# Kernel optimization log

Hardware: AMD Instinct MI355X
Metric: run time of the kernel (lower is better)

Reference implementation:

```python
import jax, jax.numpy as jnp
import numpy as np

B, A_IN, C_IN, H, W_ = 8, 16, 4, 64, 64   # batch, input atoms, input capsules, spatial
K, C_OUT, A_OUT, ROUTINGS = 5, 8, 32, 3
EPS = 1e-7


def setup_inputs() -> dict:
    key = jax.random.key(0)
    k1, k2 = jax.random.split(key)
    x = jax.random.normal(k1, (B, A_IN, C_IN, H, W_), dtype=jnp.float32)
    # kaiming_uniform_(fan_in, relu): bound = sqrt(3) * sqrt(2) / sqrt(fan_in)
    fan_in = A_IN * K * K
    bound = float(np.sqrt(6.0 / fan_in))
    W = jax.random.uniform(k2, (C_OUT * A_OUT, A_IN, K, K), jnp.float32, -bound, bound)
    b = jnp.full((1, 1, C_OUT, A_OUT), 0.1, dtype=jnp.float32)
    return {"x": x, "W": W, "b": b}


def _squash(v):
    # v: (..., atoms); SegCaps squash with epsilon inside sqrt
    sq = jnp.sum(v * v, axis=-1, keepdims=True)
    return v * (sq / (1.0 + sq) / jnp.sqrt(sq + EPS))


def reference(x, W, b):
    # Faithful to torch: permute then raw row-major reshapes (byte reinterpret)
    t = jnp.transpose(x, (2, 0, 3, 4, 1))                      # (C_IN, B, H, W, A_IN)
    t = t.reshape(C_IN * B, H, W_, A_IN).reshape(-1, A_IN, H, W_)
    conv = jax.lax.conv_general_dilated(
        t, W, window_strides=(1, 1), padding="SAME",
        dimension_numbers=("NCHW", "OIHW", "NCHW"))             # (C_IN*B, C_OUT*A_OUT, h, w)
    ch, cw = conv.shape[2], conv.shape[3]
    votes = conv.reshape(B, C_IN, ch, cw, C_OUT, A_OUT)         # raw reinterpret, as in torch
    biases = jnp.tile(b, (ch, cw, 1, 1))                        # (h, w, C_OUT, A_OUT)

    # dynamic routing (SegCaps update_routing)
    logits = jnp.zeros((B, C_IN, ch, cw, C_OUT), dtype=votes.dtype)
    activation = None
    for _ in range(ROUTINGS):
        route = jax.nn.softmax(logits, axis=-1)                 # (B, Cin, h, w, Cout)
        preact = jnp.einsum("bihwo,bihwoa->bhwoa", route, votes) + biases
        activation = _squash(preact)                            # (B, h, w, Cout, A)
        agreement = jnp.einsum("bihwoa,bhwoa->bihwo", votes, activation)
        logits = logits + agreement
    return jnp.transpose(activation, (0, 4, 3, 1, 2))           # (B, A_OUT, C_OUT, h, w)
```

## Files before the change

kernel.cpp:

```cpp
#include <hip/hip_runtime.h>
#include <hip/hip_bf16.h>


typedef _Float16 half8 __attribute__((ext_vector_type(8)));
typedef _Float16 half4v __attribute__((ext_vector_type(4)));
typedef float floatx4 __attribute__((ext_vector_type(4)));

#define EPSF 1e-7f

__global__ __launch_bounds__(256) void k_pack2(const float* __restrict__ x,
                                               _Float16* __restrict__ th) {
  __shared__ float lin[32 * 306 + 18];
  const int bid = blockIdx.x;
  const int n   = bid >> 3;
  const int a0h = (bid >> 2) & 1;
  const int W0  = (bid & 3) * 16;
  const int ci = n >> 3, b0 = n & 7;
  const int tid = threadIdx.x;
  const float* xb = x + b0 * 262144 + ci * 4096 + W0;

  for (int p = 0; p < 8; ++p) {
    int rr = p * 64 + (tid >> 2);
    int q  = (tid & 3) * 4;
    int a1 = rr >> 5, m = rr & 31;
    float4 v = *(const float4*)(xb + a1 * 16384 + (a0h * 32 + m) * 64 + q);
    float* d = lin + m * 306 + a1 * 18 + q;
    d[0] = v.x; d[1] = v.y; d[2] = v.z; d[3] = v.w;
  }
  __syncthreads();

  _Float16* tb = th + (size_t)n * 65536 + a0h * 32768 + W0 * 128;
  for (int hh = 0; hh < 4; ++hh) {
    int w1 = tid >> 4, a1 = tid & 15;
    half8 v;
#pragma unroll
    for (int j = 0; j < 8; ++j)
      v[j] = (_Float16)lin[(j * 4 + hh) * 306 + a1 * 18 + w1];
    *(half8*)(tb + hh * 8192 + w1 * 128 + a1 * 8) = v;
  }
}

__global__ __launch_bounds__(256) void k_packw(const float* __restrict__ W,
                                               _Float16* __restrict__ Wp) {
  int id = blockIdx.x * 256 + threadIdx.x;
  int a  = id & 15;
  int oc = (id >> 4) & 255;
  int kk = id >> 12;
  Wp[id] = (kk < 25) ? (_Float16)W[oc * 400 + a * 25 + kk] : (_Float16)0.0f;
}

__global__ __launch_bounds__(256) void k_conv(const _Float16* __restrict__ th,
                                              const _Float16* __restrict__ Wp,
                                              _Float16* __restrict__ votes) {
  __shared__ _Float16 lds[5440];
  const int y = blockIdx.x;
  const int n = blockIdx.y;
  const int tid = threadIdx.x;

  for (int c = tid; c < 680; c += 256) {
    int a0h = c / 340;
    int rem = c - a0h * 340;
    int r   = rem / 68;
    int col = rem - r * 68;
    int row = y + r - 2;
    half8 v = {};
    if (col >= 2 && col <= 65 && row >= 0 && row < 64)
      v = *(const half8*)(th + (size_t)(((n * 2 + a0h) * 64 + row) * 64 + (col - 2)) * 8);
    *(half8*)(lds + c * 8) = v;
  }
  __syncthreads();

  const int lane  = tid & 63;
  const int wv    = tid >> 6;
  const int col16 = lane & 15;
  const int quad  = lane >> 4;
  const int t     = quad >> 1;
  const int a0h   = quad & 1;
  const int m0    = wv * 64;

  floatx4 acc[4][4] = {};

  const _Float16* wbase = Wp + (size_t)t * 4096 + (m0 + col16) * 16 + a0h * 8;
  half8 af[4], an[4], bf[4];
#pragma unroll
  for (int oct = 0; oct < 4; ++oct)
    af[oct] = *(const half8*)(wbase + oct * 256);

  for (int s = 0; s < 13; ++s) {
    int kkb = 2 * s + t; if (kkb > 24) kkb = 24;
    int ky = kkb / 5;
    int kx = kkb - ky * 5;
    const _Float16* lb = lds + (a0h * 340 + ky * 68 + col16 + kx) * 8;
#pragma unroll
    for (int xt = 0; xt < 4; ++xt)
      bf[xt] = *(const half8*)(lb + xt * 128);
    int sn = (s + 1 < 13) ? (s + 1) : s;
#pragma unroll
    for (int oct = 0; oct < 4; ++oct)
      an[oct] = *(const half8*)(wbase + (size_t)sn * 8192 + oct * 256);
#pragma unroll
    for (int oct = 0; oct < 4; ++oct)
#pragma unroll
      for (int xt = 0; xt < 4; ++xt)
        acc[oct][xt] = __builtin_amdgcn_mfma_f32_16x16x32_f16(
            af[oct], bf[xt], acc[oct][xt], 0, 0, 0);
#pragma unroll
    for (int oct = 0; oct < 4; ++oct) af[oct] = an[oct];
  }

  _Float16* vbase = votes + (size_t)n * 1048576 + y * 64;
#pragma unroll
  for (int oct = 0; oct < 4; ++oct)
#pragma unroll
    for (int xt = 0; xt < 4; ++xt)
#pragma unroll
      for (int r = 0; r < 4; ++r) {
        int oc = m0 + oct * 16 + quad * 4 + r;
        int xx = xt * 16 + col16;
        vbase[(size_t)oc * 4096 + xx] = (_Float16)acc[oct][xt][r];
      }
}

__global__ __launch_bounds__(256) void k_routing2(
    const _Float16* __restrict__ votes, const float* __restrict__ bias,
    float* __restrict__ out) {
  __shared__ float so[256 * 36];
  const int tid  = threadIdx.x;
  const int lane = tid & 63;
  const int wv   = tid >> 6;
  const int bid  = blockIdx.x;
  const int bv = bid >> 7;
  const int h  = (bid >> 1) & 63;
  const int W0 = (bid & 1) * 32;

  float4 bia = *(const float4*)(bias + lane * 4);
  const int o  = lane >> 3;
  const int a0 = (lane & 7) * 4;

  for (int k = 0; k < 8; ++k) {
    const int wl = wv * 8 + k;
    const int w  = W0 + wl;
    const _Float16* vb = votes + (size_t)bv * 4194304 + h * 16384 + w * 256 + lane * 4;
    float4 v[4];
#pragma unroll
    for (int i = 0; i < 4; ++i) {
      half4v hv = *(const half4v*)(vb + (size_t)i * 1048576);
      v[i] = make_float4((float)hv.x, (float)hv.y, (float)hv.z, (float)hv.w);
    }

    float logit[4] = {0.f, 0.f, 0.f, 0.f};
    float act[4];

#pragma unroll
    for (int r = 0; r < 3; ++r) {
      float route[4];
#pragma unroll
      for (int i = 0; i < 4; ++i) {
        float m = logit[i];
        m = fmaxf(m, __shfl_xor(m, 8, 64));
        m = fmaxf(m, __shfl_xor(m, 16, 64));
        m = fmaxf(m, __shfl_xor(m, 32, 64));
        float e = __expf(logit[i] - m);
        float s = e;
        s += __shfl_xor(s, 8, 64);
        s += __shfl_xor(s, 16, 64);
        s += __shfl_xor(s, 32, 64);
        route[i] = e / s;
      }
      float pr[4] = {bia.x, bia.y, bia.z, bia.w};
#pragma unroll
      for (int i = 0; i < 4; ++i) {
        pr[0] = fmaf(route[i], v[i].x, pr[0]);
        pr[1] = fmaf(route[i], v[i].y, pr[1]);
        pr[2] = fmaf(route[i], v[i].z, pr[2]);
        pr[3] = fmaf(route[i], v[i].w, pr[3]);
      }
      float sq = pr[0]*pr[0] + pr[1]*pr[1] + pr[2]*pr[2] + pr[3]*pr[3];
      sq += __shfl_xor(sq, 1, 64);
      sq += __shfl_xor(sq, 2, 64);
      sq += __shfl_xor(sq, 4, 64);
      float scale = sq / (1.f + sq) / sqrtf(sq + EPSF);
#pragma unroll
      for (int j = 0; j < 4; ++j) act[j] = pr[j] * scale;

      if (r < 2) {
#pragma unroll
        for (int i = 0; i < 4; ++i) {
          float ag = v[i].x*act[0] + v[i].y*act[1] + v[i].z*act[2] + v[i].w*act[3];
          ag += __shfl_xor(ag, 1, 64);
          ag += __shfl_xor(ag, 2, 64);
          ag += __shfl_xor(ag, 4, 64);
          logit[i] += ag;
        }
      }
    }

#pragma unroll
    for (int j = 0; j < 4; ++j)
      so[((a0 + j) * 8 + o) * 36 + wl] = act[j];
  }
  __syncthreads();

  float* ob = out + (size_t)bv * 1048576 + h * 64 + W0;
  for (int p = 0; p < 8; ++p) {
    int r  = p * 32 + (tid >> 3);
    int w0 = (tid & 7) * 4;
    float4 v = *(const float4*)(so + r * 36 + w0);
    *(float4*)(ob + (size_t)r * 4096 + w0) = v;
  }
}

extern "C" void kernel_launch(void* const* d_in, const int* in_sizes, int n_in,
                              void* d_out, int out_size, void* d_ws, size_t ws_size,
                              hipStream_t stream) {
  const float* x  = (const float*)d_in[0];
  const float* W  = (const float*)d_in[1];
  const float* b  = (const float*)d_in[2];
  float* out = (float*)d_out;

  _Float16* th    = (_Float16*)d_ws;
  _Float16* Wp    = th + 2097152;
  _Float16* votes = Wp + 106496;

  k_pack2<<<256, 256, 0, stream>>>(x, th);
  k_packw<<<416, 256, 0, stream>>>(W, Wp);
  k_conv<<<dim3(64, 32), 256, 0, stream>>>(th, Wp, votes);
  k_routing2<<<1024, 256, 0, stream>>>(votes, b, out);
}
```

Baseline: 147.1 us.

## Stage conv output through LDS and speed up routing reductions with DPP/permlane

The conv kernel now writes its accumulators into a swizzled LDS tile, then emits 16-byte coalesced stores of votes instead of scattered 2-byte stores. The routing kernel replaces shuffle-based reductions with DPP and permlane swap instructions, and evaluates the first iteration in closed form using uniform routes of 1/8. It also uses fast reciprocal and rsqrt intrinsics and swizzles the output LDS staging to avoid bank conflicts. In exchange it adds LDS traffic and an extra barrier in conv, relies on inline asm specific to gfx950, and takes a small precision hit from the approximate reciprocal and rsqrt.

```diff
diff --git a/kernel.cpp b/kernel.cpp
--- a/kernel.cpp
+++ b/kernel.cpp
@@ -7,6 +7,38 @@
 typedef float floatx4 __attribute__((ext_vector_type(4)));
 
 #define EPSF 1e-7f
+
+template <int CTRL>
+__device__ __forceinline__ float dppmov(float x) {
+  return __int_as_float(__builtin_amdgcn_update_dpp(
+      0, __float_as_int(x), CTRL, 0xf, 0xf, false));
+}
+__device__ __forceinline__ float red_a_add(float x) {
+  x += dppmov<0xB1>(x);
+  x += dppmov<0x4E>(x);
+  x += dppmov<0x141>(x);
+  return x;
+}
+__device__ __forceinline__ float red_o_add(float x) {
+  x += dppmov<0x128>(x);
+  { float a = x, b = x;
+    asm("v_permlane16_swap_b32 %0, %1" : "+v"(a), "+v"(b));
+    x = a + b; }
+  { float a = x, b = x;
+    asm("v_permlane32_swap_b32 %0, %1" : "+v"(a), "+v"(b));
+    x = a + b; }
+  return x;
+}
+__device__ __forceinline__ float red_o_max(float x) {
+  x = fmaxf(x, dppmov<0x128>(x));
+  { float a = x, b = x;
+    asm("v_permlane16_swap_b32 %0, %1" : "+v"(a), "+v"(b));
+    x = fmaxf(a, b); }
+  { float a = x, b = x;
+    asm("v_permlane32_swap_b32 %0, %1" : "+v"(a), "+v"(b));
+    x = fmaxf(a, b); }
+  return x;
+}
 
 __global__ __launch_bounds__(256) void k_pack2(const float* __restrict__ x,
                                                _Float16* __restrict__ th) {
@@ -52,7 +84,7 @@
 __global__ __launch_bounds__(256) void k_conv(const _Float16* __restrict__ th,
                                               const _Float16* __restrict__ Wp,
                                               _Float16* __restrict__ votes) {
-  __shared__ _Float16 lds[5440];
+  __shared__ _Float16 lds[16384];
   const int y = blockIdx.x;
   const int n = blockIdx.y;
   const int tid = threadIdx.x;
@@ -108,7 +140,7 @@
     for (int oct = 0; oct < 4; ++oct) af[oct] = an[oct];
   }
 
-  _Float16* vbase = votes + (size_t)n * 1048576 + y * 64;
+  __syncthreads();
 #pragma unroll
   for (int oct = 0; oct < 4; ++oct)
 #pragma unroll
@@ -117,11 +149,23 @@
       for (int r = 0; r < 4; ++r) {
         int oc = m0 + oct * 16 + quad * 4 + r;
         int xx = xt * 16 + col16;
-        vbase[(size_t)oc * 4096 + xx] = (_Float16)acc[oct][xt][r];
+        int sw = (oc & 15) >> 1;
+        lds[oc * 64 + (xx ^ (sw << 3))] = (_Float16)acc[oct][xt][r];
       }
-}
-
-__global__ __launch_bounds__(256) void k_routing2(
+  __syncthreads();
+  _Float16* vb2 = votes + (size_t)n * 1048576 + y * 64;
+#pragma unroll
+  for (int it = 0; it < 8; ++it) {
+    int idx = it * 256 + tid;
+    int oc  = idx >> 3;
+    int x0  = (idx & 7) << 3;
+    int sw  = (oc & 15) >> 1;
+    half8 hv = *(const half8*)(lds + oc * 64 + (x0 ^ (sw << 3)));
+    *(half8*)(vb2 + (size_t)oc * 4096 + x0) = hv;
+  }
+}
+
+__global__ __launch_bounds__(256) void k_routing3(
     const _Float16* __restrict__ votes, const float* __restrict__ bias,
     float* __restrict__ out) {
   __shared__ float so[256 * 36];
@@ -134,79 +178,90 @@
   const int W0 = (bid & 1) * 32;
 
   float4 bia = *(const float4*)(bias + lane * 4);
-  const int o  = lane >> 3;
-  const int a0 = (lane & 7) * 4;
+  const int o     = lane >> 3;
+  const int a0    = (lane & 7) * 4;
+  const int shift = a0 >> 2;
+  float bb[4] = {bia.x, bia.y, bia.z, bia.w};
 
   for (int k = 0; k < 8; ++k) {
     const int wl = wv * 8 + k;
     const int w  = W0 + wl;
     const _Float16* vb = votes + (size_t)bv * 4194304 + h * 16384 + w * 256 + lane * 4;
-    float4 v[4];
+    float v[4][4];
 #pragma unroll
     for (int i = 0; i < 4; ++i) {
       half4v hv = *(const half4v*)(vb + (size_t)i * 1048576);
-      v[i] = make_float4((float)hv.x, (float)hv.y, (float)hv.z, (float)hv.w);
-    }
-
-    float logit[4] = {0.f, 0.f, 0.f, 0.f};
-    float act[4];
-
-#pragma unroll
-    for (int r = 0; r < 3; ++r) {
+#pragma unroll
+      for (int j = 0; j < 4; ++j) v[i][j] = (float)hv[j];
+    }
+
+    float logit[4], act[4], pr[4];
+
+#pragma unroll
+    for (int j = 0; j < 4; ++j)
+      pr[j] = fmaf(0.125f, (v[0][j] + v[1][j]) + (v[2][j] + v[3][j]), bb[j]);
+    {
+      float sq = pr[0]*pr[0] + pr[1]*pr[1] + pr[2]*pr[2] + pr[3]*pr[3];
+      sq = red_a_add(sq);
+      float sc = sq * __builtin_amdgcn_rcpf(1.f + sq)
+                    * __builtin_amdgcn_rsqf(sq + EPSF);
+#pragma unroll
+      for (int j = 0; j < 4; ++j) act[j] = pr[j] * sc;
+    }
+#pragma unroll
+    for (int i = 0; i < 4; ++i) {
+      float ag = v[i][0]*act[0] + v[i][1]*act[1] + v[i][2]*act[2] + v[i][3]*act[3];
+      logit[i] = red_a_add(ag);
+    }
+
+#pragma unroll
+    for (int r = 1; r < 3; ++r) {
       float route[4];
 #pragma unroll
       for (int i = 0; i < 4; ++i) {
-        float m = logit[i];
-        m = fmaxf(m, __shfl_xor(m, 8, 64));
-        m = fmaxf(m, __shfl_xor(m, 16, 64));
-        m = fmaxf(m, __shfl_xor(m, 32, 64));
+        float m = red_o_max(logit[i]);
         float e = __expf(logit[i] - m);
-        float s = e;
-        s += __shfl_xor(s, 8, 64);
-        s += __shfl_xor(s, 16, 64);
-        s += __shfl_xor(s, 32, 64);
-        route[i] = e / s;
+        float s = red_o_add(e);
+        route[i] = e * __builtin_amdgcn_rcpf(s);
       }
-      float pr[4] = {bia.x, bia.y, bia.z, bia.w};
-#pragma unroll
-      for (int i = 0; i < 4; ++i) {
-        pr[0] = fmaf(route[i], v[i].x, pr[0]);
-        pr[1] = fmaf(route[i], v[i].y, pr[1]);
-        pr[2] = fmaf(route[i], v[i].z, pr[2]);
-        pr[3] = fmaf(route[i], v[i].w, pr[3]);
-      }
+#pragma unroll
+      for (int j = 0; j < 4; ++j) pr[j] = bb[j];
+#pragma unroll
+      for (int i = 0; i < 4; ++i)
+#pragma unroll
+        for (int j = 0; j < 4; ++j)
+          pr[j] = fmaf(route[i], v[i][j], pr[j]);
       float sq = pr[0]*pr[0] + pr[1]*pr[1] + pr[2]*pr[2] + pr[3]*pr[3];
-      sq += __shfl_xor(sq, 1, 64);
-      sq += __shfl_xor(sq, 2, 64);
-      sq += __shfl_xor(sq, 4, 64);
-      float scale = sq / (1.f + sq) / sqrtf(sq + EPSF);
-#pragma unroll
-      for (int j = 0; j < 4; ++j) act[j] = pr[j] * scale;
-
+      sq = red_a_add(sq);
+      float sc = sq * __builtin_amdgcn_rcpf(1.f + sq)
+                    * __builtin_amdgcn_rsqf(sq + EPSF);
+#pragma unroll
+      for (int j = 0; j < 4; ++j) act[j] = pr[j] * sc;
       if (r < 2) {
 #pragma unroll
         for (int i = 0; i < 4; ++i) {
-          float ag = v[i].x*act[0] + v[i].y*act[1] + v[i].z*act[2] + v[i].w*act[3];
-          ag += __shfl_xor(ag, 1, 64);
-          ag += __shfl_xor(ag, 2, 64);
-          ag += __shfl_xor(ag, 4, 64);
-          logit[i] += ag;
+          float ag = v[i][0]*act[0] + v[i][1]*act[1] + v[i][2]*act[2] + v[i][3]*act[3];
+          logit[i] += red_a_add(ag);
         }
       }
     }
 
 #pragma unroll
     for (int j = 0; j < 4; ++j)
-      so[((a0 + j) * 8 + o) * 36 + wl] = act[j];
+      so[((a0 + j) * 8 + o) * 36 + (wl ^ shift)] = act[j];
   }
   __syncthreads();
 
   float* ob = out + (size_t)bv * 1048576 + h * 64 + W0;
+#pragma unroll
   for (int p = 0; p < 8; ++p) {
     int r  = p * 32 + (tid >> 3);
     int w0 = (tid & 7) * 4;
-    float4 v = *(const float4*)(so + r * 36 + w0);
-    *(float4*)(ob + (size_t)r * 4096 + w0) = v;
+    float4 tv = *(const float4*)(so + r * 36 + (w0 ^ (p & 4)));
+    float tt[4] = {tv.x, tv.y, tv.z, tv.w};
+    const int pm = p & 3;
+    float4 u = make_float4(tt[0 ^ pm], tt[1 ^ pm], tt[2 ^ pm], tt[3 ^ pm]);
+    *(float4*)(ob + (size_t)r * 4096 + w0) = u;
   }
 }
 
@@ -225,5 +280,5 @@
   k_pack2<<<256, 256, 0, stream>>>(x, th);
   k_packw<<<416, 256, 0, stream>>>(W, Wp);
   k_conv<<<dim3(64, 32), 256, 0, stream>>>(th, Wp, votes);
-  k_routing2<<<1024, 256, 0, stream>>>(votes, b, out);
-}
+  k_routing3<<<1024, 256, 0, stream>>>(votes, b, out);
+}
```

Result: faster. 139.4 us (-5.2%).
